# Kernel tuning notes

Hardware: AMD Instinct MI355X
Metric: run time of the kernel (lower is better)

Reference implementation:

```python
import jax, jax.numpy as jnp
import numpy as np

IN, OUT, E, R = 2048, 2048, 8, 8

def setup_inputs() -> dict:
    key = jax.random.key(0)
    ks = jax.random.split(key, 8)
    B, S = 4, 2048
    x = jax.random.normal(ks[0], (B, S, IN), dtype=jnp.float32)
    routing_weights = jax.random.uniform(ks[1], (B, E), dtype=jnp.float32)
    W = jax.random.normal(ks[2], (OUT, IN), dtype=jnp.float32) / np.sqrt(IN).astype(np.float32)
    b = jax.random.normal(ks[3], (OUT,), dtype=jnp.float32) * 0.01
    lora_A_s = jax.random.normal(ks[4], (IN, R), dtype=jnp.float32) / np.sqrt(IN).astype(np.float32)
    lora_B_s = jax.random.normal(ks[5], (R, OUT), dtype=jnp.float32) * 0.01
    lora_A_e = jax.random.normal(ks[6], (E, IN, R), dtype=jnp.float32) / np.sqrt(IN).astype(np.float32)
    lora_B_e = jax.random.normal(ks[7], (E, R, OUT), dtype=jnp.float32) * 0.01
    return {"x": x, "routing_weights": routing_weights, "W": W, "b": b,
            "lora_A_s": lora_A_s, "lora_B_s": lora_B_s,
            "lora_A_e": lora_A_e, "lora_B_e": lora_B_e}

def reference(x, routing_weights, W, b, lora_A_s, lora_B_s, lora_A_e, lora_B_e):
    # base linear: [B,S,IN] @ [IN,OUT] + [OUT]
    base_out = jnp.einsum('bsi,oi->bso', x, W) + b
    # shared low-rank path
    shared_out = (x @ lora_A_s) @ lora_B_s
    # all experts batched: t[b,s,e,r] = x @ A_e[e]; weighted reduce over experts
    t = jnp.einsum('bsi,eir->bser', x, lora_A_e)          # [B,S,E,R]
    expert_out = jnp.einsum('bser,ero,be->bso', t, lora_B_e, routing_weights)
    return base_out + shared_out + expert_out
```

## Files before the change

kernel.cpp:

```cpp
#include <hip/hip_runtime.h>
#include <hip/hip_bf16.h>

#define IN_DIM 2048
#define OUT_DIM 2048
#define NE 8
#define M_TOT 8192
#define NB 4
#define RK 96

typedef short short8 __attribute__((ext_vector_type(8)));
typedef float floatx4 __attribute__((ext_vector_type(4)));
typedef unsigned short us;

__device__ __forceinline__ us f2bf(float f) {
    __hip_bfloat16 h = __float2bfloat16(f);
    return *reinterpret_cast<us*>(&h);
}

__device__ __forceinline__ short8 cvt8(float4 v0, float4 v1) {
    short8 o;
    o[0] = (short)f2bf(v0.x); o[1] = (short)f2bf(v0.y);
    o[2] = (short)f2bf(v0.z); o[3] = (short)f2bf(v0.w);
    o[4] = (short)f2bf(v1.x); o[5] = (short)f2bf(v1.y);
    o[6] = (short)f2bf(v1.z); o[7] = (short)f2bf(v1.w);
    return o;
}

__device__ __forceinline__ void gld_lds16(const void* g, void* l) {
    __builtin_amdgcn_global_load_lds(
        (const __attribute__((address_space(1))) void*)g,
        (__attribute__((address_space(3))) void*)l, 16, 0, 0);
}


template <int KX>
__device__ __forceinline__ void stage2(const us* src, char* lds) {
    gld_lds16(src, lds);
    gld_lds16(src + 128 * KX, lds + 8192);
}

__device__ __forceinline__ void mfma_quad(floatx4 (&acc)[8][4], const short8 (&af)[4],
                                          const short8 (&bf)[4], int mq) {
#pragma unroll
    for (int i = 0; i < 4; ++i)
#pragma unroll
        for (int ni = 0; ni < 4; ++ni)
            acc[mq * 4 + i][ni] =
                __builtin_amdgcn_mfma_f32_16x16x32_bf16(af[i], bf[ni], acc[mq * 4 + i][ni], 0, 0, 0);
}

template <int KX, int SM, int VM0, int VM2, bool RD3>
__device__ __forceinline__ void ktile(
    const us* __restrict__ pA, const us* __restrict__ pB, int k1, int k2,
    const char* smC, const char* smN, char* lwC, char* lwN,
    int ab, int bb,
    short8 (&afA)[4], short8 (&afB)[4], short8 (&bfA)[4], short8 (&bfB)[4],
    floatx4 (&acc)[8][4])
{
#pragma unroll
    for (int i = 0; i < 4; ++i) afB[i] = *(const short8*)(smC + ab + (4 + i) * 1024);
    asm volatile("s_waitcnt lgkmcnt(4)" ::: "memory");
    __builtin_amdgcn_sched_barrier(0);
    __builtin_amdgcn_s_setprio(1);
    mfma_quad(acc, afA, bfA, 0);
    __builtin_amdgcn_s_setprio(0);
    if (SM & 1) stage2<KX>(pA + k1 + 32, lwN + 32768);
    if (VM0 == 8)      asm volatile("s_waitcnt vmcnt(8)" ::: "memory");
    else if (VM0 == 0) asm volatile("s_waitcnt vmcnt(0)" ::: "memory");
    __builtin_amdgcn_s_barrier();

#pragma unroll
    for (int i = 0; i < 4; ++i) afA[i] = *(const short8*)(smC + 32768 + ab + (4 + i) * 1024);
#pragma unroll
    for (int i = 0; i < 4; ++i) bfB[i] = *(const short8*)(smC + 32768 + bb + i * 1024);
    asm volatile("s_waitcnt lgkmcnt(8)" ::: "memory");
    __builtin_amdgcn_sched_barrier(0);
    __builtin_amdgcn_s_setprio(1);
    mfma_quad(acc, afB, bfA, 1);
    __builtin_amdgcn_s_setprio(0);
    if (SM & 2) stage2<KX>(pB + k2, lwC + 16384);
    __builtin_amdgcn_s_barrier();

#pragma unroll
    for (int i = 0; i < 4; ++i) afB[i] = *(const short8*)(smC + 32768 + ab + i * 1024);
    asm volatile("s_waitcnt lgkmcnt(4)" ::: "memory");
    __builtin_amdgcn_sched_barrier(0);
    __builtin_amdgcn_s_setprio(1);
    mfma_quad(acc, afA, bfB, 1);
    __builtin_amdgcn_s_setprio(0);
    if (SM & 4) stage2<KX>(pA + k2, lwC);
    if (VM2 == 8)      asm volatile("s_waitcnt vmcnt(8)" ::: "memory");
    else if (VM2 == 4) asm volatile("s_waitcnt vmcnt(4)" ::: "memory");
    __builtin_amdgcn_s_barrier();

    if (RD3) {
#pragma unroll
        for (int i = 0; i < 4; ++i) afA[i] = *(const short8*)(smN + ab + i * 1024);
#pragma unroll
        for (int i = 0; i < 4; ++i) bfA[i] = *(const short8*)(smN + bb + i * 1024);
        asm volatile("s_waitcnt lgkmcnt(8)" ::: "memory");
    } else {
        asm volatile("s_waitcnt lgkmcnt(0)" ::: "memory");
    }
    __builtin_amdgcn_sched_barrier(0);
    __builtin_amdgcn_s_setprio(1);
    mfma_quad(acc, afB, bfB, 0);
    __builtin_amdgcn_s_setprio(0);
    if (SM & 8) stage2<KX>(pB + k2 + 32, lwC + 49152);
    __builtin_amdgcn_s_barrier();
}

template <int KX, bool PB>
__global__ __launch_bounds__(512) void main_gemm_t(const us* __restrict__ A,
                                                   const us* __restrict__ Bw,
                                                   const float* __restrict__ bias,
                                                   float* __restrict__ out) {
    extern __shared__ char smem[];
    constexpr int NT = KX / 64;
    int tid = threadIdx.x;
    int lane = tid & 63, w = tid >> 6;
    int wm = w >> 2, wn = w & 3;
    int rlo = lane & 15, kq = lane >> 4;

    int b = blockIdx.x;
    int bs = (b & 7) * 32 + (b >> 3);
    int m0 = (bs >> 3) * 256, n0 = (bs & 7) * 256;

    const us* B = PB ? (Bw + (size_t)(m0 >> 11) * OUT_DIM * KX) : Bw;

    int swz = (kq ^ ((rlo >> 1) & 3)) * 16;
    int ab = (wm * 128 + rlo) * 64 + swz;
    int bb = 16384 + (wn * 64 + rlo) * 64 + swz;

    int r0 = tid >> 2;
    int ps = tid & 3;
    int ssw = (ps ^ ((r0 >> 1) & 3)) * 8;
    const us* pA = A + (size_t)(m0 + r0) * KX + ssw;
    const us* pB = B + (size_t)(n0 + r0) * KX + ssw;
    char* lw0 = smem + w * 1024;
    char* lw1 = lw0 + 65536;
    const char* sm0 = smem;
    const char* sm1 = smem + 65536;

    floatx4 acc[8][4];
#pragma unroll
    for (int mi = 0; mi < 8; ++mi)
#pragma unroll
        for (int ni = 0; ni < 4; ++ni) acc[mi][ni] = (floatx4)0.f;

    stage2<KX>(pA,      lw0);
    stage2<KX>(pB,      lw0 + 16384);
    stage2<KX>(pA + 32, lw0 + 32768);
    stage2<KX>(pB + 32, lw0 + 49152);
    stage2<KX>(pA + 64, lw1);
    stage2<KX>(pB + 64, lw1 + 16384);
    stage2<KX>(pB + 96, lw1 + 49152);
    asm volatile("s_waitcnt vmcnt(10)" ::: "memory");
    __builtin_amdgcn_s_barrier();

    short8 afA[4], afB[4], bfA[4], bfB[4];
#pragma unroll
    for (int i = 0; i < 4; ++i) afA[i] = *(const short8*)(sm0 + ab + i * 1024);
#pragma unroll
    for (int i = 0; i < 4; ++i) bfA[i] = *(const short8*)(sm0 + bb + i * 1024);

    for (int tt = 0; tt < NT / 2 - 1; ++tt) {
        int t0 = tt * 2;
        ktile<KX, 0xF, 8, 8, true>(pA, pB, (t0 + 1) * 64, (t0 + 2) * 64,
                                   sm0, sm1, lw0, lw1, ab, bb, afA, afB, bfA, bfB, acc);
        ktile<KX, 0xF, 8, 8, true>(pA, pB, (t0 + 2) * 64, (t0 + 3) * 64,
                                   sm1, sm0, lw1, lw0, ab, bb, afA, afB, bfA, bfB, acc);
    }
    ktile<KX, 0x1, 8, 4, true>(pA, pB, (NT - 1) * 64, NT * 64,
                               sm0, sm1, lw0, lw1, ab, bb, afA, afB, bfA, bfB, acc);
    ktile<KX, 0x0, 0, -1, false>(pA, pB, 0, 0,
                                 sm1, sm0, lw1, lw0, ab, bb, afA, afB, bfA, bfB, acc);

    float bbias[4];
#pragma unroll
    for (int ni = 0; ni < 4; ++ni) bbias[ni] = bias[n0 + wn * 64 + ni * 16 + rlo];
#pragma unroll
    for (int mi = 0; mi < 8; ++mi) {
        int row = m0 + wm * 128 + mi * 16 + kq * 4;
#pragma unroll
        for (int ni = 0; ni < 4; ++ni) {
            int col = n0 + wn * 64 + ni * 16 + rlo;
#pragma unroll
            for (int r = 0; r < 4; ++r)
                out[(size_t)(row + r) * OUT_DIM + col] = acc[mi][ni][r] + bbias[ni];
        }
    }
}


__global__ __launch_bounds__(512) void prep_combo(
    const float* __restrict__ x, const float* __restrict__ As,
    const float* __restrict__ Ae, const float* __restrict__ Bs,
    const float* __restrict__ Be, const float* __restrict__ rw,
    us* __restrict__ Aext, us* __restrict__ AcatI, us* __restrict__ BcatT)
{
    int bid = blockIdx.x;
    int tid = threadIdx.x;

    if (bid < 512) {
        int half = tid >> 8;
        int col = (tid & 255) * 8;
#pragma unroll 8
        for (int pass = 0; pass < 8; ++pass) {
            int row = bid * 16 + pass * 2 + half;
            const float4* src = (const float4*)(x + (size_t)row * IN_DIM + col);
            *(short8*)(Aext + (size_t)row * IN_DIM + col) = cvt8(src[0], src[1]);
        }
    } else if (bid < 544) {
        if (tid < 64) {
            int r = (bid - 512) * 64 + tid;
            us* dst = AcatI + (size_t)r * RK;
            const float4* as = (const float4*)(As + (size_t)r * 8);
            *(short8*)dst = cvt8(as[0], as[1]);
#pragma unroll
            for (int e = 0; e < 8; ++e) {
                const float4* ae = (const float4*)(Ae + ((size_t)e * IN_DIM + r) * 8);
                *(short8*)(dst + 8 + e * 8) = cvt8(ae[0], ae[1]);
            }
            short8 z = (short8)0;
            *(short8*)(dst + 72) = z; *(short8*)(dst + 80) = z; *(short8*)(dst + 88) = z;
        }
    } else {
        int n = (bid - 544) * 512 + tid;
        float com[72];
#pragma unroll
        for (int rp = 0; rp < 8; ++rp)  com[rp] = Bs[(size_t)rp * OUT_DIM + n];
#pragma unroll
        for (int rp = 8; rp < 72; ++rp) com[rp] = Be[(size_t)(rp - 8) * OUT_DIM + n];
#pragma unroll
        for (int bb = 0; bb < NB; ++bb) {
            us v[RK];
#pragma unroll
            for (int rp = 0; rp < 8; ++rp)  v[rp] = f2bf(com[rp]);
#pragma unroll
            for (int rp = 8; rp < 72; ++rp) v[rp] = f2bf(com[rp] * rw[bb * NE + ((rp - 8) >> 3)]);
#pragma unroll
            for (int rp = 72; rp < 96; ++rp) v[rp] = 0;
            us* dst = BcatT + ((size_t)bb * OUT_DIM + n) * RK;
#pragma unroll
            for (int j = 0; j < 12; ++j)
                *(short8*)(dst + j * 8) = *(short8*)(v + j * 8);
        }
    }
}

__global__ __launch_bounds__(512) void delta_wb(const float* __restrict__ W,
                                                const us* __restrict__ AcatI,
                                                const us* __restrict__ BcatT,
                                                us* __restrict__ Bext) {
    int tid = threadIdx.x;
    int lane = tid & 63, w = tid >> 6;
    int wm = w >> 2, wn = w & 3;
    int rlo = lane & 15, kq = lane >> 4;
    int b = blockIdx.x >> 6;
    int t6 = blockIdx.x & 63;
    int nn0 = (t6 >> 3) * 256, ii0 = (t6 & 7) * 256;

    const us* bct = BcatT + ((size_t)b * OUT_DIM + nn0 + wm * 128 + rlo) * RK + kq * 8;
    const us* aci = AcatI + ((size_t)(ii0 + wn * 64 + rlo)) * RK + kq * 8;

    floatx4 acc[8][4];
#pragma unroll
    for (int mi = 0; mi < 8; ++mi)
#pragma unroll
        for (int ni = 0; ni < 4; ++ni) acc[mi][ni] = (floatx4)0.f;

#pragma unroll
    for (int ks = 0; ks < 3; ++ks) {
        int k0 = ks * 32;
        short8 af[8], bf[4];
#pragma unroll
        for (int mi = 0; mi < 8; ++mi)
            af[mi] = *(const short8*)(bct + (size_t)mi * 16 * RK + k0);
#pragma unroll
        for (int ni = 0; ni < 4; ++ni)
            bf[ni] = *(const short8*)(aci + (size_t)ni * 16 * RK + k0);
#pragma unroll
        for (int mi = 0; mi < 8; ++mi)
#pragma unroll
            for (int ni = 0; ni < 4; ++ni)
                acc[mi][ni] = __builtin_amdgcn_mfma_f32_16x16x32_bf16(
                    af[mi], bf[ni], acc[mi][ni], 0, 0, 0);
    }

#pragma unroll
    for (int mi = 0; mi < 8; ++mi) {
#pragma unroll
        for (int r = 0; r < 4; ++r) {
            int n = nn0 + wm * 128 + mi * 16 + kq * 4 + r;
#pragma unroll
            for (int ni = 0; ni < 4; ++ni) {
                int i = ii0 + wn * 64 + ni * 16 + rlo;
                float val = acc[mi][ni][r] + W[(size_t)n * IN_DIM + i];
                Bext[((size_t)b * OUT_DIM + n) * IN_DIM + i] = f2bf(val);
            }
        }
    }
}

#define K_EXT1 2176
#define RANK_PAD 128

__global__ void prep_wb_fb(const float* __restrict__ W, const float* __restrict__ Bs,
                           const float* __restrict__ Be, const float* __restrict__ As,
                           const float* __restrict__ Ae, us* __restrict__ Bext,
                           us* __restrict__ AcatT) {
    int blk = blockIdx.x;
    int t = threadIdx.x;
    if (blk < OUT_DIM) {
        int n = blk;
        const float4* src = (const float4*)(W + (size_t)n * IN_DIM + t * 8);
        *(short8*)(Bext + (size_t)n * K_EXT1 + t * 8) = cvt8(src[0], src[1]);
        if (t < RANK_PAD) {
            float v = 0.f;
            if (t < 8)       v = Bs[(size_t)t * OUT_DIM + n];
            else if (t < 72) v = Be[(size_t)(t - 8) * OUT_DIM + n];
            Bext[(size_t)n * K_EXT1 + IN_DIM + t] = f2bf(v);
        }
    } else {
        int kp = blk - OUT_DIM;
        int i0 = t * 8;
        short8 o;
#pragma unroll
        for (int j = 0; j < 8; ++j) {
            int i = i0 + j;
            float v = 0.f;
            if (kp < 8)       v = As[(size_t)i * 8 + kp];
            else if (kp < 72) v = Ae[(size_t)((kp - 8) >> 3) * IN_DIM * 8 + (size_t)i * 8 + ((kp - 8) & 7)];
            o[j] = (short)f2bf(v);
        }
        *(short8*)(AcatT + (size_t)kp * IN_DIM + i0) = o;
    }
}

__global__ __launch_bounds__(512) void tgemm_fused_fb(const float* __restrict__ x,
                                                      us* __restrict__ Aext,
                                                      const us* __restrict__ AcatT,
                                                      const float* __restrict__ routing) {
    __shared__ floatx4 red[8][64][6];
    int tid = threadIdx.x;
    int lane = tid & 63, w = tid >> 6;
    int rlo = lane & 15, kq = lane >> 4;
    int mbase = blockIdx.x * 16;

    floatx4 acc[6];
#pragma unroll
    for (int ni = 0; ni < 6; ++ni) acc[ni] = (floatx4)0.f;

    const float* xrow = x + (size_t)(mbase + rlo) * IN_DIM + w * 256 + kq * 8;
    us* arow = Aext + (size_t)(mbase + rlo) * K_EXT1 + w * 256 + kq * 8;
    const us* bbase = AcatT + (size_t)rlo * IN_DIM + w * 256 + kq * 8;

#pragma unroll
    for (int kt = 0; kt < 8; ++kt) {
        int k0 = kt * 32;
        float4 v0 = *(const float4*)(xrow + k0);
        float4 v1 = *(const float4*)(xrow + k0 + 4);
        short8 a = cvt8(v0, v1);
        *(short8*)(arow + k0) = a;
#pragma unroll
        for (int ni = 0; ni < 6; ++ni) {
            short8 bfr = *(const short8*)(bbase + (size_t)(ni * 16) * IN_DIM + k0);
            acc[ni] = __builtin_amdgcn_mfma_f32_16x16x32_bf16(a, bfr, acc[ni], 0, 0, 0);
        }
    }

#pragma unroll
    for (int ni = 0; ni < 6; ++ni) red[w][lane][ni] = acc[ni];
    __syncthreads();
    if (w == 0) {
#pragma unroll
        for (int ni = 0; ni < 6; ++ni) {
            floatx4 s = red[0][lane][ni];
#pragma unroll
            for (int ww = 1; ww < 8; ++ww) s += red[ww][lane][ni];
            int col = ni * 16 + rlo;
#pragma unroll
            for (int r = 0; r < 4; ++r) {
                int row = mbase + kq * 4 + r;
                float fac = (col < 8) ? 1.f
                          : (col < 72 ? routing[(row >> 11) * NE + ((col - 8) >> 3)] : 0.f);
                Aext[(size_t)row * K_EXT1 + IN_DIM + col] = f2bf(s[r] * fac);
            }
        }
#pragma unroll
        for (int c = 0; c < 2; ++c) {
            int col = 96 + c * 16 + rlo;
#pragma unroll
            for (int r = 0; r < 4; ++r)
                Aext[(size_t)(mbase + kq * 4 + r) * K_EXT1 + IN_DIM + col] = 0;
        }
    }
}

extern "C" void kernel_launch(void* const* d_in, const int* in_sizes, int n_in,
                              void* d_out, int out_size, void* d_ws, size_t ws_size,
                              hipStream_t stream) {
    const float* x   = (const float*)d_in[0];
    const float* rw  = (const float*)d_in[1];
    const float* W   = (const float*)d_in[2];
    const float* bv  = (const float*)d_in[3];
    const float* As  = (const float*)d_in[4];
    const float* Bs  = (const float*)d_in[5];
    const float* Ae  = (const float*)d_in[6];
    const float* Be  = (const float*)d_in[7];
    float* out = (float*)d_out;

    size_t pA  = 0;
    size_t pB  = pA + (size_t)M_TOT * IN_DIM * 2;
    size_t pAI = pB + (size_t)NB * OUT_DIM * IN_DIM * 2;
    size_t pBT = pAI + (size_t)IN_DIM * RK * 2;
    size_t need2 = pBT + (size_t)NB * OUT_DIM * RK * 2;

    if (ws_size >= need2) {
        us* Aext  = (us*)((char*)d_ws + pA);
        us* Bext  = (us*)((char*)d_ws + pB);
        us* AcatI = (us*)((char*)d_ws + pAI);
        us* BcatT = (us*)((char*)d_ws + pBT);

        hipFuncSetAttribute((const void*)&main_gemm_t<2048, true>,
                            hipFuncAttributeMaxDynamicSharedMemorySize, 131072);

        prep_combo<<<548, 512, 0, stream>>>(x, As, Ae, Bs, Be, rw, Aext, AcatI, BcatT);
        delta_wb<<<256, 512, 0, stream>>>(W, AcatI, BcatT, Bext);
        main_gemm_t<2048, true><<<256, 512, 131072, stream>>>(Aext, Bext, bv, out);
        return;
    }

    size_t fA = 0;
    size_t fB = fA + (size_t)M_TOT * K_EXT1 * 2;
    size_t fC = fB + (size_t)OUT_DIM * K_EXT1 * 2;
    size_t need1 = fC + (size_t)96 * IN_DIM * 2;
    if (ws_size < need1) return;

    us* Aext  = (us*)((char*)d_ws + fA);
    us* Bext  = (us*)((char*)d_ws + fB);
    us* AcatT = (us*)((char*)d_ws + fC);

    hipFuncSetAttribute((const void*)&main_gemm_t<2176, false>,
                        hipFuncAttributeMaxDynamicSharedMemorySize, 131072);

    prep_wb_fb<<<OUT_DIM + 96, 256, 0, stream>>>(W, Bs, Be, As, Ae, Bext, AcatT);
    tgemm_fused_fb<<<M_TOT / 16, 512, 0, stream>>>(x, Aext, AcatT, rw);
    main_gemm_t<2176, false><<<256, 512, 131072, stream>>>(Aext, Bext, bv, out);
}
```

Before: 116.3 us.

## Rebalance prep kernels: move x conversion into delta kernel, simplify GEMM tile order

Splits the small LoRA factor preparation into its own tiny kernel and moves the large x-to-bf16 conversion into the same launch as the per-batch weight-delta GEMM. The two independent jobs can then overlap on the GPU instead of the heavy conversion sitting before the delta GEMM. The main GEMM's block-to-tile mapping also changes from a swizzled order to a plain row-major order, which alters L2 reuse of A and B tiles across concurrently running blocks.

```diff
diff --git a/kernel.cpp b/kernel.cpp
--- a/kernel.cpp
+++ b/kernel.cpp
@@ -123,8 +123,8 @@
     int rlo = lane & 15, kq = lane >> 4;
 
     int b = blockIdx.x;
-    int bs = (b & 7) * 32 + (b >> 3);
-    int m0 = (bs >> 3) * 256, n0 = (bs & 7) * 256;
+    int n0 = (b & 7) * 256;
+    int m0 = (b >> 3) * 256;
 
     const us* B = PB ? (Bw + (size_t)(m0 >> 11) * OUT_DIM * KX) : Bw;
 
@@ -192,28 +192,16 @@
     }
 }
 
-
-__global__ __launch_bounds__(512) void prep_combo(
-    const float* __restrict__ x, const float* __restrict__ As,
-    const float* __restrict__ Ae, const float* __restrict__ Bs,
-    const float* __restrict__ Be, const float* __restrict__ rw,
-    us* __restrict__ Aext, us* __restrict__ AcatI, us* __restrict__ BcatT)
+__global__ __launch_bounds__(256) void tiny_prep(
+    const float* __restrict__ As, const float* __restrict__ Ae,
+    const float* __restrict__ Bs, const float* __restrict__ Be,
+    const float* __restrict__ rw, us* __restrict__ AcatI, us* __restrict__ BcatT)
 {
     int bid = blockIdx.x;
     int tid = threadIdx.x;
-
-    if (bid < 512) {
-        int half = tid >> 8;
-        int col = (tid & 255) * 8;
-#pragma unroll 8
-        for (int pass = 0; pass < 8; ++pass) {
-            int row = bid * 16 + pass * 2 + half;
-            const float4* src = (const float4*)(x + (size_t)row * IN_DIM + col);
-            *(short8*)(Aext + (size_t)row * IN_DIM + col) = cvt8(src[0], src[1]);
-        }
-    } else if (bid < 544) {
+    if (bid < 32) {
         if (tid < 64) {
-            int r = (bid - 512) * 64 + tid;
+            int r = bid * 64 + tid;
             us* dst = AcatI + (size_t)r * RK;
             const float4* as = (const float4*)(As + (size_t)r * 8);
             *(short8*)dst = cvt8(as[0], as[1]);
@@ -226,7 +214,7 @@
             *(short8*)(dst + 72) = z; *(short8*)(dst + 80) = z; *(short8*)(dst + 88) = z;
         }
     } else {
-        int n = (bid - 544) * 512 + tid;
+        int n = (bid - 32) * 256 + tid;
         float com[72];
 #pragma unroll
         for (int rp = 0; rp < 8; ++rp)  com[rp] = Bs[(size_t)rp * OUT_DIM + n];
@@ -249,16 +237,32 @@
     }
 }
 
-__global__ __launch_bounds__(512) void delta_wb(const float* __restrict__ W,
-                                                const us* __restrict__ AcatI,
-                                                const us* __restrict__ BcatT,
-                                                us* __restrict__ Bext) {
+__global__ __launch_bounds__(512) void combo(
+    const float* __restrict__ x, const float* __restrict__ W,
+    const us* __restrict__ AcatI, const us* __restrict__ BcatT,
+    us* __restrict__ Aext, us* __restrict__ Bext)
+{
+    int bid = blockIdx.x;
     int tid = threadIdx.x;
+
+    if (bid >= 256) {
+        int xb = bid - 256;
+        int half = tid >> 8;
+        int col = (tid & 255) * 8;
+#pragma unroll 8
+        for (int pass = 0; pass < 8; ++pass) {
+            int row = xb * 16 + pass * 2 + half;
+            const float4* src = (const float4*)(x + (size_t)row * IN_DIM + col);
+            *(short8*)(Aext + (size_t)row * IN_DIM + col) = cvt8(src[0], src[1]);
+        }
+        return;
+    }
+
     int lane = tid & 63, w = tid >> 6;
     int wm = w >> 2, wn = w & 3;
     int rlo = lane & 15, kq = lane >> 4;
-    int b = blockIdx.x >> 6;
-    int t6 = blockIdx.x & 63;
+    int b = bid >> 6;
+    int t6 = bid & 63;
     int nn0 = (t6 >> 3) * 256, ii0 = (t6 & 7) * 256;
 
     const us* bct = BcatT + ((size_t)b * OUT_DIM + nn0 + wm * 128 + rlo) * RK + kq * 8;
@@ -426,8 +430,8 @@
         hipFuncSetAttribute((const void*)&main_gemm_t<2048, true>,
                             hipFuncAttributeMaxDynamicSharedMemorySize, 131072);
 
-        prep_combo<<<548, 512, 0, stream>>>(x, As, Ae, Bs, Be, rw, Aext, AcatI, BcatT);
-        delta_wb<<<256, 512, 0, stream>>>(W, AcatI, BcatT, Bext);
+        tiny_prep<<<40, 256, 0, stream>>>(As, Ae, Bs, Be, rw, AcatI, BcatT);
+        combo<<<768, 512, 0, stream>>>(x, W, AcatI, BcatT, Aext, Bext);
         main_gemm_t<2048, true><<<256, 512, 131072, stream>>>(Aext, Bext, bv, out);
         return;
     }
```

Result: faster. 112.6 us (-3.2%).
